# Kernel tuning notes

Measured on AMD Instinct MI355X. Metric: run time of the kernel, lower is better.

## Reference

```python
import jax, jax.numpy as jnp
import numpy as np

N, E, H, IN_NF, G, STEPS, EHID = 4096, 8192, 128, 64, 8, 3, 32


def setup_inputs() -> dict:
    key = jax.random.key(0)
    ks = jax.random.split(key, 24)

    def gn(k, shape, fan_in):
        return jax.random.normal(k, shape, dtype=jnp.float32) / np.sqrt(fan_in)

    inp = {
        "x": jax.random.normal(ks[0], (N, IN_NF), dtype=jnp.float32),
        "edge_index": jax.random.randint(ks[1], (2, E), 0, N, dtype=jnp.int32),
        "edge_attr": jax.random.uniform(ks[2], (E, 1), dtype=jnp.float32),
        "batch": jnp.sort(jax.random.randint(ks[3], (N,), 0, G, dtype=jnp.int32)),
        # lin0: in_nf -> hid
        "lin0_w": gn(ks[4], (IN_NF, H), IN_NF),
        "lin0_b": jnp.zeros((H,), jnp.float32),
        # per-step edge MLP: 1 -> 32 -> H*H (stacked over STEPS)
        "nn_w1": gn(ks[5], (STEPS, 1, EHID), 1),
        "nn_b1": jnp.zeros((STEPS, EHID), jnp.float32),
        "nn_w2": gn(ks[6], (STEPS, EHID, H * H), EHID) * 0.1,
        "nn_b2": jnp.zeros((STEPS, H * H), jnp.float32),
        # NNConv root weight (no bias) + conv bias, per step
        "root_w": gn(ks[7], (STEPS, H, H), H),
        "conv_b": jnp.zeros((STEPS, H), jnp.float32),
        # single-layer GRU (input H, hidden H); gate order r, z, n
        "gru_wih": gn(ks[8], (3 * H, H), H),
        "gru_whh": gn(ks[9], (3 * H, H), H),
        "gru_bih": jnp.zeros((3 * H,), jnp.float32),
        "gru_bhh": jnp.zeros((3 * H,), jnp.float32),
        # readout
        "lin1_w": gn(ks[10], (H, H // 2), H),
        "lin1_b": jnp.zeros((H // 2,), jnp.float32),
        "lin2_w": gn(ks[11], (H // 2, 1), H // 2),
        "lin2_b": jnp.zeros((1,), jnp.float32),
    }
    return inp


def _gru_cell(m, h, wih, whh, bih, bhh):
    gi = m @ wih.T + bih          # [N, 3H]
    gh = h @ whh.T + bhh          # [N, 3H]
    i_r, i_z, i_n = jnp.split(gi, 3, axis=-1)
    h_r, h_z, h_n = jnp.split(gh, 3, axis=-1)
    r = jax.nn.sigmoid(i_r + h_r)
    z = jax.nn.sigmoid(i_z + h_z)
    n = jnp.tanh(i_n + r * h_n)
    return (1.0 - z) * n + z * h


def reference(x, edge_index, edge_attr, batch, lin0_w, lin0_b, nn_w1, nn_b1,
              nn_w2, nn_b2, root_w, conv_b, gru_wih, gru_whh, gru_bih,
              gru_bhh, lin1_w, lin1_b, lin2_w, lin2_b):
    n_nodes = x.shape[0]
    row, col = edge_index[0], edge_index[1]  # source j -> target i

    x = jax.nn.relu(x @ lin0_w + lin0_b)     # [N, H]
    h = x

    # in-degree for mean aggregation (0-degree nodes -> 0 output)
    deg = jax.ops.segment_sum(jnp.ones((row.shape[0],), x.dtype), col,
                              num_segments=n_nodes)
    inv_deg = jnp.where(deg > 0, 1.0 / jnp.maximum(deg, 1.0), 0.0)[:, None]

    for t in range(STEPS):
        # edge-conditioned weights: [E, H, H]
        e_h = jax.nn.relu(edge_attr @ nn_w1[t] + nn_b1[t])
        w_e = (e_h @ nn_w2[t] + nn_b2[t]).reshape(-1, H, H)
        # gather -> per-edge matvec -> scatter-mean
        msg = jnp.einsum('eh,eho->eo', x[row], w_e)
        agg = jax.ops.segment_sum(msg, col, num_segments=n_nodes) * inv_deg
        m = jax.nn.relu(agg + x @ root_w[t] + conv_b[t])
        h = _gru_cell(m, h, gru_wih, gru_whh, gru_bih, gru_bhh)
        x = h

    # global mean pool over graphs
    cnt = jax.ops.segment_sum(jnp.ones((n_nodes,), x.dtype), batch,
                              num_segments=G)
    g = jax.ops.segment_sum(x, batch, num_segments=G) / jnp.maximum(cnt, 1.0)[:, None]
    g = jax.nn.relu(g @ lin1_w + lin1_b)  # dropout: eval mode (identity)
    out = g @ lin2_w + lin2_b             # [G, 1]
    return out
```

## Files before the change

### kernel.cpp

```cpp
#include <hip/hip_runtime.h>
#include <math.h>

#define NN 4096
#define EE 8192
#define HH 128
#define GG 8
#define MU 4096

typedef __attribute__((ext_vector_type(8))) _Float16 half8;
typedef __attribute__((ext_vector_type(4))) float floatx4;

__device__ __forceinline__ void ldst16(const _Float16* g, void* l) {
    __builtin_amdgcn_global_load_lds(
        (const __attribute__((address_space(1))) unsigned int*)g,
        (__attribute__((address_space(3))) unsigned int*)l, 16, 0, 0);
}

__device__ __forceinline__ unsigned f2u(float f) {
    unsigned b = __float_as_uint(f);
    return (b & 0x80000000u) ? ~b : (b | 0x80000000u);
}
__device__ __forceinline__ float u2f(unsigned u) {
    return __uint_as_float((u & 0x80000000u) ? (u ^ 0x80000000u) : ~u);
}

__device__ __forceinline__ int cls_k(float w, float b, float mn, float mx) {
    const float hi = w > 0.f ? w * mx + b : w * mn + b;
    const float lo = w > 0.f ? w * mn + b : w * mx + b;
    if (hi <= 0.f) return 0;
    if (lo >= 0.f) return 1;
    return 2;
}

__global__ __launch_bounds__(256) void ymix_gh_k(
    const _Float16* __restrict__ A, const _Float16* __restrict__ BT3t,
    const _Float16* __restrict__ Bhh, const float* __restrict__ bhh,
    const float* __restrict__ w2t, _Float16* __restrict__ Y,
    float* __restrict__ g2, _Float16* __restrict__ U,
    const int* __restrict__ kflag)
{
    __shared__ __align__(16) _Float16 As[128 * 32];
    __shared__ __align__(16) _Float16 Bs[128 * 32];
    const int tid = threadIdx.x;
    const int lane = tid & 63, wave = tid >> 6;
    const int m0 = blockIdx.y * 128;
    const int wr = (wave >> 1) * 64, wc = (wave & 1) * 64;
    const int fm = lane & 15, fq = lane >> 4;
    const int srow = tid >> 2, soff = (tid & 3) << 3;
    const _Float16* gA0 = A + (size_t)(m0 + srow) * 128 + soff;
    const _Float16* gA1 = gA0 + (size_t)64 * 128;
    char* lA0 = (char*)As + tid * 16;  char* lA1 = (char*)As + (tid + 256) * 16;
    char* lB0 = (char*)Bs + tid * 16;  char* lB1 = (char*)Bs + (tid + 256) * 16;
    const int bx = blockIdx.x;
    const int er = fq * 4, ec = fm;

    floatx4 acc[4][4] = {};
    if (bx < 6) {
        const _Float16* gB0 = (bx < 3)
            ? BT3t + (size_t)(bx * 128 + srow) * 128 + soff
            : Bhh + (size_t)((bx - 3) * 128 + srow) * 128 + soff;
        const _Float16* gB1 = gB0 + (size_t)64 * 128;
        for (int k0 = 0; k0 < 128; k0 += 32) {
            __syncthreads();
            ldst16(gA0 + k0, lA0); ldst16(gA1 + k0, lA1);
            ldst16(gB0 + k0, lB0); ldst16(gB1 + k0, lB1);
            __syncthreads();
            half8 af[4], bf[4];
#pragma unroll
            for (int i = 0; i < 4; ++i)
                af[i] = *(const half8*)&As[(wr + i * 16 + fm) * 32 + fq * 8];
#pragma unroll
            for (int j = 0; j < 4; ++j)
                bf[j] = *(const half8*)&Bs[(wc + j * 16 + fm) * 32 + fq * 8];
#pragma unroll
            for (int i = 0; i < 4; ++i)
#pragma unroll
                for (int j = 0; j < 4; ++j)
                    acc[i][j] = __builtin_amdgcn_mfma_f32_16x16x32_f16(
                        af[i], bf[j], acc[i][j], 0, 0, 0);
        }
        if (bx < 3) {
#pragma unroll
            for (int i = 0; i < 4; ++i) {
                const int gr = m0 + wr + i * 16 + er;
#pragma unroll
                for (int j = 0; j < 4; ++j) {
                    const int gc = bx * 128 + wc + j * 16 + ec;
#pragma unroll
                    for (int r = 0; r < 4; ++r)
                        Y[(size_t)(gr + r) * 384 + gc] = (_Float16)acc[i][j][r];
                }
            }
        } else {
            const int n0 = (bx - 3) * 128;
#pragma unroll
            for (int i = 0; i < 4; ++i) {
                const int gr = m0 + wr + i * 16 + er;
#pragma unroll
                for (int j = 0; j < 4; ++j) {
                    const int gc = n0 + wc + j * 16 + ec;
                    const float bv = bhh[gc];
#pragma unroll
                    for (int r = 0; r < 4; ++r)
                        g2[(size_t)(gr + r) * 384 + gc] = acc[i][j][r] + bv;
                }
            }
        }
    } else {
        const unsigned f = *(const unsigned*)kflag;
        const int kk = bx - 6;
        if (!((f >> kk) & 1u)) return;
        const int cbase = __popc(f & ((1u << kk) - 1u)) << 7;
        const float* w2s = w2t + (size_t)kk * 16384;
        for (int k0 = 0; k0 < 128; k0 += 32) {
            __syncthreads();
            ldst16(gA0 + k0, lA0); ldst16(gA1 + k0, lA1);
#pragma unroll
            for (int c = tid; c < 512; c += 256) {
                const int row = c >> 2, seg = (c & 3) << 3;
                _Float16 v8[8];
#pragma unroll
                for (int u = 0; u < 8; ++u)
                    v8[u] = (_Float16)w2s[(size_t)(k0 + seg + u) * 128 + row];
                *(half8*)&Bs[row * 32 + seg] = *(half8*)v8;
            }
            __syncthreads();
            half8 af[4], bf[4];
#pragma unroll
            for (int i = 0; i < 4; ++i)
                af[i] = *(const half8*)&As[(wr + i * 16 + fm) * 32 + fq * 8];
#pragma unroll
            for (int j = 0; j < 4; ++j)
                bf[j] = *(const half8*)&Bs[(wc + j * 16 + fm) * 32 + fq * 8];
#pragma unroll
            for (int i = 0; i < 4; ++i)
#pragma unroll
                for (int j = 0; j < 4; ++j)
                    acc[i][j] = __builtin_amdgcn_mfma_f32_16x16x32_f16(
                        af[i], bf[j], acc[i][j], 0, 0, 0);
        }
#pragma unroll
        for (int i = 0; i < 4; ++i) {
            const int gr = m0 + wr + i * 16 + er;
#pragma unroll
            for (int j = 0; j < 4; ++j) {
                const int gc = cbase + wc + j * 16 + ec;
#pragma unroll
                for (int r = 0; r < 4; ++r)
                    U[(size_t)(gr + r) * MU + gc] = (_Float16)acc[i][j][r];
            }
        }
    }
}

__global__ __launch_bounds__(256) void escat_k(
    const int2* __restrict__ rc, const float2* __restrict__ ec2,
    const float* __restrict__ ehPt, const _Float16* __restrict__ Y,
    const _Float16* __restrict__ U, float* __restrict__ mpre,
    const int* __restrict__ kflag)
{
    const int b = blockIdx.x;
    const int p0 = ((b & 7) * 512 + (b >> 3)) * 2;
    const int h2 = threadIdx.x >> 7;
    const int o = threadIdx.x & 127;
    const int p = p0 + h2;
    const int2 e = rc[p];
    const float2 c = ec2[p];
    const _Float16* Yr = Y + (size_t)e.x * 384;
    float acc = c.x * (float)Yr[o] + c.y * (float)Yr[128 + o];
    const unsigned f = *(const unsigned*)kflag;
    if (f) {
        const int nk = __popc(f);
        const _Float16* Ur = U + (size_t)e.x * MU;
        const float* ep = ehPt + (size_t)p * 32;
        for (int i = 0; i < nk; ++i)
            acc += ep[i] * (float)Ur[i * 128 + o];
    }
    atomicAdd(&mpre[(size_t)e.y * 128 + o], acc);
}

__global__ __launch_bounds__(256) void gruz0_k(
    const float* __restrict__ mpre, const _Float16* __restrict__ Y,
    const float* __restrict__ cb, const _Float16* __restrict__ Bih,
    const float* __restrict__ bih, float* __restrict__ g1)
{
    __shared__ __align__(16) _Float16 As[128 * 40];
    __shared__ __align__(16) _Float16 Bs[128 * 40];
    const int tid = threadIdx.x;
    const int lane = tid & 63, wave = tid >> 6;
    const int m0 = blockIdx.y * 128, n0 = blockIdx.x * 128;
    const int wr = (wave >> 1) * 64, wc = (wave & 1) * 64;
    const int fm = lane & 15, fq = lane >> 4;

    floatx4 acc[4][4] = {};
    for (int k0 = 0; k0 < 128; k0 += 32) {
        __syncthreads();
#pragma unroll
        for (int c = tid; c < 512; c += 256) {
            const int row = c >> 2, seg = (c & 3) << 3;
            const int mr = m0 + row;
            const half8 yv = *(const half8*)&Y[(size_t)mr * 384 + 256 + k0 + seg];
            const float4 a0 = *(const float4*)&mpre[(size_t)mr * 128 + k0 + seg];
            const float4 a1 = *(const float4*)&mpre[(size_t)mr * 128 + k0 + seg + 4];
            const float4 c0 = *(const float4*)&cb[k0 + seg];
            const float4 c1 = *(const float4*)&cb[k0 + seg + 4];
            _Float16 v8[8];
            float v;
            v = (float)yv[0] + a0.x + c0.x; v8[0] = (_Float16)(v > 0.f ? v : 0.f);
            v = (float)yv[1] + a0.y + c0.y; v8[1] = (_Float16)(v > 0.f ? v : 0.f);
            v = (float)yv[2] + a0.z + c0.z; v8[2] = (_Float16)(v > 0.f ? v : 0.f);
            v = (float)yv[3] + a0.w + c0.w; v8[3] = (_Float16)(v > 0.f ? v : 0.f);
            v = (float)yv[4] + a1.x + c1.x; v8[4] = (_Float16)(v > 0.f ? v : 0.f);
            v = (float)yv[5] + a1.y + c1.y; v8[5] = (_Float16)(v > 0.f ? v : 0.f);
            v = (float)yv[6] + a1.z + c1.z; v8[6] = (_Float16)(v > 0.f ? v : 0.f);
            v = (float)yv[7] + a1.w + c1.w; v8[7] = (_Float16)(v > 0.f ? v : 0.f);
            *(half8*)&As[row * 40 + seg] = *(half8*)v8;
            *(half8*)&Bs[row * 40 + seg] =
                *(const half8*)&Bih[(size_t)(n0 + row) * 128 + k0 + seg];
        }
        __syncthreads();
        half8 af[4], bf[4];
#pragma unroll
        for (int i = 0; i < 4; ++i)
            af[i] = *(const half8*)&As[(wr + i * 16 + fm) * 40 + fq * 8];
#pragma unroll
        for (int j = 0; j < 4; ++j)
            bf[j] = *(const half8*)&Bs[(wc + j * 16 + fm) * 40 + fq * 8];
#pragma unroll
        for (int i = 0; i < 4; ++i)
#pragma unroll
            for (int j = 0; j < 4; ++j)
                acc[i][j] = __builtin_amdgcn_mfma_f32_16x16x32_f16(
                    af[i], bf[j], acc[i][j], 0, 0, 0);
    }
    const int er = fq * 4, ec = fm;
#pragma unroll
    for (int i = 0; i < 4; ++i) {
        const int gr = m0 + wr + i * 16 + er;
#pragma unroll
        for (int j = 0; j < 4; ++j) {
            const int gc = n0 + wc + j * 16 + ec;
            const float bv = bih[gc];
#pragma unroll
            for (int r = 0; r < 4; ++r)
                g1[(size_t)(gr + r) * 384 + gc] = acc[i][j][r] + bv;
        }
    }
}

__global__ void gate_k(const float* __restrict__ G1, const float* __restrict__ G2,
                       float* __restrict__ xh, _Float16* __restrict__ Ax,
                       const int* __restrict__ batch, float* __restrict__ pooled) {
    const int idx = blockIdx.x * 256 + threadIdx.x;
    const int n = idx >> 7, o = idx & 127;
    const size_t b = (size_t)n * 384;
    float ir = G1[b + o], iz = G1[b + 128 + o], in_ = G1[b + 256 + o];
    float hr = G2[b + o], hz = G2[b + 128 + o], hn = G2[b + 256 + o];
    float r = 1.f / (1.f + expf(-(ir + hr)));
    float z = 1.f / (1.f + expf(-(iz + hz)));
    float nv = tanhf(in_ + r * hn);
    float hv = (1.f - z) * nv + z * xh[idx];
    xh[idx] = hv;
    Ax[idx] = (_Float16)hv;
    if (pooled) atomicAdd(&pooled[batch[n] * 128 + o], hv);
}

__global__ __launch_bounds__(256) void setup_lin0_k(
    const float* __restrict__ wih, const float* __restrict__ whh,
    _Float16* __restrict__ Bih, _Float16* __restrict__ Bhh,
    const int* __restrict__ ei, const float* __restrict__ eattr,
    const int* __restrict__ batch,
    float* __restrict__ deg, int* __restrict__ odeg, float* __restrict__ cnt,
    unsigned* __restrict__ eaMM,
    const float* __restrict__ x, const float* __restrict__ l0w,
    const float* __restrict__ l0b, float* __restrict__ xh,
    _Float16* __restrict__ Ax)
{
    __shared__ float loc8[GG];
    __shared__ float As[16][64];
    __shared__ float Bs[16][64];
    const int b = blockIdx.x, t = threadIdx.x;
    if (b < 192) {
        const int idx = b * 256 + t;
        Bih[idx] = (_Float16)wih[idx];
        Bhh[idx] = (_Float16)whh[idx];
    } else if (b < 224) {
        const int e = (b - 192) * 256 + t;
        atomicAdd(&deg[ei[EE + e]], 1.0f);
        atomicAdd(&odeg[ei[e]], 1);
        const float ea = eattr[e];
        unsigned u1 = f2u(ea), u2 = f2u(-ea);
#pragma unroll
        for (int off = 32; off > 0; off >>= 1) {
            unsigned o1 = __shfl_down(u1, off), o2 = __shfl_down(u2, off);
            u1 = u1 > o1 ? u1 : o1;  u2 = u2 > o2 ? u2 : o2;
        }
        if ((t & 63) == 0) { atomicMax(&eaMM[0], u1); atomicMax(&eaMM[1], u2); }
    } else if (b < 240) {
        const int n = (b - 224) * 256 + t;
        if (t < GG) loc8[t] = 0.f;
        __syncthreads();
        atomicAdd(&loc8[batch[n]], 1.0f);
        __syncthreads();
        if (t < GG) atomicAdd(&cnt[t], loc8[t]);
    } else {
        const int bb = b - 240;
        const int j0 = (bb & 1) * 64;
        const int m0 = (bb >> 1) * 64;
        const int tx = t & 15, ty = t >> 4;
        const int arow = t >> 2, acol = (t & 3) << 2;
        const int bk = t >> 4, bj = (t & 15) << 2;
        float c[4][4] = {};
        for (int k0 = 0; k0 < 64; k0 += 16) {
            __syncthreads();
            float4 av = *(const float4*)&x[(size_t)(m0 + arow) * 64 + k0 + acol];
            As[acol + 0][arow] = av.x;
            As[acol + 1][arow] = av.y;
            As[acol + 2][arow] = av.z;
            As[acol + 3][arow] = av.w;
            *(float4*)&Bs[bk][bj] = *(const float4*)&l0w[(size_t)(k0 + bk) * 128 + j0 + bj];
            __syncthreads();
#pragma unroll
            for (int kk = 0; kk < 16; ++kk) {
                const float4 a = *(const float4*)&As[kk][ty << 2];
                const float4 bv = *(const float4*)&Bs[kk][tx << 2];
                c[0][0] += a.x * bv.x; c[0][1] += a.x * bv.y; c[0][2] += a.x * bv.z; c[0][3] += a.x * bv.w;
                c[1][0] += a.y * bv.x; c[1][1] += a.y * bv.y; c[1][2] += a.y * bv.z; c[1][3] += a.y * bv.w;
                c[2][0] += a.z * bv.x; c[2][1] += a.z * bv.y; c[2][2] += a.z * bv.z; c[2][3] += a.z * bv.w;
                c[3][0] += a.w * bv.x; c[3][1] += a.w * bv.y; c[3][2] += a.w * bv.z; c[3][3] += a.w * bv.w;
            }
        }
        const float4 bv = *(const float4*)&l0b[j0 + (tx << 2)];
        const int col0 = j0 + (tx << 2);
#pragma unroll
        for (int i = 0; i < 4; ++i) {
            const int row = m0 + (ty << 2) + i;
            float4 o;
            o.x = fmaxf(c[i][0] + bv.x, 0.f); o.y = fmaxf(c[i][1] + bv.y, 0.f);
            o.z = fmaxf(c[i][2] + bv.z, 0.f); o.w = fmaxf(c[i][3] + bv.w, 0.f);
            *(float4*)&xh[(size_t)row * 128 + col0] = o;
            _Float16* base = Ax + (size_t)row * 128 + col0;
            base[0] = (_Float16)o.x; base[1] = (_Float16)o.y;
            base[2] = (_Float16)o.z; base[3] = (_Float16)o.w;
        }
    }
}

__global__ __launch_bounds__(256) void scan_wsum_k(
    const int* __restrict__ odeg, int* __restrict__ ocur,
    const float* __restrict__ w1, const float* __restrict__ b1,
    const float* __restrict__ w2, const float* __restrict__ b2,
    const float* __restrict__ rw, const unsigned* __restrict__ eaMM,
    _Float16* __restrict__ BT3)
{
    const int t = threadIdx.x;
    if (blockIdx.x == 0) {
        __shared__ int ps[256];
        const int base = t * 16;
        int l[16]; int s = 0;
#pragma unroll
        for (int i = 0; i < 16; ++i) { l[i] = s; s += odeg[base + i]; }
        ps[t] = s;
        __syncthreads();
        for (int d = 1; d < 256; d <<= 1) {
            int v = (t >= d) ? ps[t - d] : 0;
            __syncthreads();
            ps[t] += v;
            __syncthreads();
        }
        const int excl = (t == 0) ? 0 : ps[t - 1];
#pragma unroll
        for (int i = 0; i < 16; ++i) ocur[base + i] = excl + l[i];
    } else {
        __shared__ float wl[32], bl[32];
        const int bb = blockIdx.x - 1;
        const int st = bb >> 6;
        if (t < 32) {
            const float w = w1[st * 32 + t], bv = b1[st * 32 + t];
            const float mx = u2f(eaMM[0]), mn = -u2f(eaMM[1]);
            const int c = cls_k(w, bv, mn, mx);
            wl[t] = (c == 1) ? w : 0.f;
            bl[t] = (c == 1) ? bv : 0.f;
        }
        __syncthreads();
        const int idx = (bb & 63) * 256 + t;
        const int h = idx >> 7, o = idx & 127;
        const float* W2t = w2 + (size_t)st * 524288;
        float a = 0.f, c2 = 0.f;
#pragma unroll 8
        for (int j = 0; j < 32; ++j) {
            const float v = W2t[(size_t)j * 16384 + idx];
            a += wl[j] * v; c2 += bl[j] * v;
        }
        c2 += b2[(size_t)st * 16384 + idx];
        _Float16* B = BT3 + (size_t)st * 49152;
        B[(size_t)o * 128 + h]         = (_Float16)a;
        B[(size_t)(128 + o) * 128 + h] = (_Float16)c2;
        B[(size_t)(256 + o) * 128 + h] = (_Float16)rw[(size_t)st * 16384 + idx];
    }
}

__global__ __launch_bounds__(256) void scatter_k(
    const int* __restrict__ ei, const float* __restrict__ eattr,
    const float* __restrict__ w1, const float* __restrict__ b1,
    const float* __restrict__ deg, int* __restrict__ ocur,
    const unsigned* __restrict__ eaMM,
    int2* __restrict__ rc, float2* __restrict__ ec2,
    float* __restrict__ ehP, int* __restrict__ kflag)
{
    __shared__ unsigned mm[3];
    if (threadIdx.x < 3) mm[threadIdx.x] = 0u;
    __syncthreads();
    if (threadIdx.x < 96) {
        const int tt = threadIdx.x >> 5, k = threadIdx.x & 31;
        const float w = w1[tt * 32 + k], bv = b1[tt * 32 + k];
        const float mx = u2f(eaMM[0]), mn = -u2f(eaMM[1]);
        if (cls_k(w, bv, mn, mx) == 2) atomicOr(&mm[tt], 1u << k);
    }
    __syncthreads();
    const int wave = threadIdx.x >> 6, lane = threadIdx.x & 63;
    const int e = blockIdx.x * 4 + wave;
    const int r = ei[e], c = ei[EE + e];
    int pos = 0;
    if (lane == 0) pos = atomicAdd(&ocur[r], 1);
    pos = __shfl(pos, 0);
    const float d = deg[c];
    const float inv = d > 0.f ? 1.0f / d : 0.0f;
    const float ea = eattr[e];
    if (lane == 0) {
        rc[pos] = make_int2(r, c);
        ec2[pos] = make_float2(ea * inv, inv);
    }
#pragma unroll
    for (int t = 0; t < 3; ++t) {
        const unsigned m = mm[t];
        if (lane < 32 && ((m >> lane) & 1u)) {
            const float v = ea * w1[t * 32 + lane] + b1[t * 32 + lane];
            const int slot = __popc(m & ((1u << lane) - 1u));
            ehP[((size_t)t * EE + pos) * 32 + slot] = (v > 0.f ? v : 0.f) * inv;
        }
    }
    if (threadIdx.x < 3) kflag[threadIdx.x] = (int)mm[threadIdx.x];
}

__global__ __launch_bounds__(128) void final_k(
    const float* __restrict__ pooled, const float* __restrict__ cnt,
    const float* __restrict__ l1w, const float* __restrict__ l1b,
    const float* __restrict__ l2w, const float* __restrict__ l2b,
    float* __restrict__ out)
{
    __shared__ float gv[128];
    const int g = blockIdx.x, t = threadIdx.x;
    float c = cnt[g]; c = c > 1.f ? c : 1.f;
    gv[t] = pooled[g * 128 + t] / c;
    __syncthreads();
    if (t < 64) {
        float y = l1b[t];
        for (int h = 0; h < 128; ++h) y += gv[h] * l1w[h * 64 + t];
        y = y > 0.f ? y : 0.f;
        float s = y * l2w[t];
#pragma unroll
        for (int off = 32; off > 0; off >>= 1)
            s += __shfl_down(s, off);
        if (t == 0) out[g] = s + l2b[0];
    }
}

extern "C" void kernel_launch(void* const* d_in, const int* in_sizes, int n_in,
                              void* d_out, int out_size, void* d_ws, size_t ws_size,
                              hipStream_t stream) {
    const float* x      = (const float*)d_in[0];
    const int*   ei     = (const int*)d_in[1];
    const float* eattr  = (const float*)d_in[2];
    const int*   batch  = (const int*)d_in[3];
    const float* lin0_w = (const float*)d_in[4];
    const float* lin0_b = (const float*)d_in[5];
    const float* nn_w1  = (const float*)d_in[6];
    const float* nn_b1  = (const float*)d_in[7];
    const float* nn_w2  = (const float*)d_in[8];
    const float* nn_b2  = (const float*)d_in[9];
    const float* root_w = (const float*)d_in[10];
    const float* conv_b = (const float*)d_in[11];
    const float* gwih   = (const float*)d_in[12];
    const float* gwhh   = (const float*)d_in[13];
    const float* gbih   = (const float*)d_in[14];
    const float* gbhh   = (const float*)d_in[15];
    const float* l1w    = (const float*)d_in[16];
    const float* l1b    = (const float*)d_in[17];
    const float* l2w    = (const float*)d_in[18];
    const float* l2b    = (const float*)d_in[19];
    float* out = (float*)d_out;
    float* ws  = (float*)d_ws;

    float*    mpre0  = ws;
    float*    pooled = ws + 1572864;
    float*    cnt    = ws + 1573888;
    float*    deg    = ws + 1573896;
    int*      odeg   = (int*)(ws + 1577992);
    unsigned* eaMM   = (unsigned*)(ws + 1582088);
    int*      kflag  = (int*)(ws + 1582090);
    int*      ocur   = (int*)(ws + 1582096);
    int2*     rc     = (int2*)(ws + 1586192);
    float2*   ec2    = (float2*)(ws + 1602576);
    float*    ehP    = ws + 1618960;
    float*    xh     = ws + 2405392;
    float*    g1     = ws + 2929680;
    float*    g2     = ws + 4502544;
    _Float16* Y      = (_Float16*)(ws + 6075408);
    _Float16* U      = (_Float16*)(ws + 6861840);
    _Float16* Ax     = (_Float16*)(ws + 15250448);
    _Float16* BT3    = (_Float16*)(ws + 15512592);
    _Float16* Bih16  = (_Float16*)(ws + 15586320);
    _Float16* Bhh16  = (_Float16*)(ws + 15610896);

    hipMemsetAsync(mpre0, 0, 6328384, stream);
    setup_lin0_k<<<368, 256, 0, stream>>>(gwih, gwhh, Bih16, Bhh16, ei, eattr,
                                          batch, deg, odeg, cnt, eaMM,
                                          x, lin0_w, lin0_b, xh, Ax);
    scan_wsum_k<<<193, 256, 0, stream>>>(odeg, ocur, nn_w1, nn_b1, nn_w2,
                                         nn_b2, root_w, eaMM, BT3);
    scatter_k<<<2048, 256, 0, stream>>>(ei, eattr, nn_w1, nn_b1, deg, ocur,
                                        eaMM, rc, ec2, ehP, kflag);

    for (int t = 0; t < 3; ++t) {
        float* mpre = mpre0 + (size_t)t * 524288;
        ymix_gh_k<<<dim3(38, 32), 256, 0, stream>>>(
            Ax, BT3 + (size_t)t * 49152, Bhh16, gbhh,
            nn_w2 + (size_t)t * 524288, Y, g2, U, kflag + t);
        escat_k<<<4096, 256, 0, stream>>>(rc, ec2, ehP + (size_t)t * EE * 32,
                                          Y, U, mpre, kflag + t);
        gruz0_k<<<dim3(3, 32), 256, 0, stream>>>(mpre, Y, conv_b + t * 128,
                                                 Bih16, gbih, g1);
        gate_k<<<2048, 256, 0, stream>>>(g1, g2, xh, Ax, batch,
                                         (t == 2) ? pooled : nullptr);
    }

    final_k<<<GG, 128, 0, stream>>>(pooled, cnt, l1w, l1b, l2w, l2b, out);
}
```

Baseline: 215.0 us.

## Fuse per-step GRU message-passing kernels into one persistent kernel with grid barriers

Replaces the 13 per-step launches (ymix_gh, escat, gruz0, gate, final) with a single persistent mega-kernel that loops over the three steps, uses grid-stride work distribution, and separates phases with an atomic-counter grid barrier. It also zeroes mpre inside the kernel instead of with a large memset. The goal is to remove launch overhead and inter-kernel gaps, at the cost of spin-barrier overhead, reduced parallelism in small phases, and a deadlock risk if not all blocks are co-resident. The grid size comes from an occupancy query, capped at 4 blocks per unit, and assumes 256 compute units.

```diff
diff --git a/kernel.cpp b/kernel.cpp
--- a/kernel.cpp
+++ b/kernel.cpp
@@ -32,237 +32,278 @@
     return 2;
 }
 
-__global__ __launch_bounds__(256) void ymix_gh_k(
-    const _Float16* __restrict__ A, const _Float16* __restrict__ BT3t,
-    const _Float16* __restrict__ Bhh, const float* __restrict__ bhh,
-    const float* __restrict__ w2t, _Float16* __restrict__ Y,
-    float* __restrict__ g2, _Float16* __restrict__ U,
-    const int* __restrict__ kflag)
+__device__ __forceinline__ void gbar(unsigned* bar, unsigned target) {
+    __syncthreads();
+    if (threadIdx.x == 0) {
+        __threadfence();
+        atomicAdd(bar, 1u);
+        while (atomicAdd(bar, 0u) < target)
+            __builtin_amdgcn_s_sleep(2);
+        __threadfence();
+    }
+    __syncthreads();
+}
+
+__global__ __launch_bounds__(256) void mega_k(
+    const int2* __restrict__ rc, const float2* __restrict__ ec2,
+    const float* __restrict__ ehP, const _Float16* __restrict__ BT3,
+    const _Float16* __restrict__ Bih, const _Float16* __restrict__ Bhh,
+    const float* __restrict__ bih, const float* __restrict__ bhh,
+    const float* __restrict__ conv_b, const float* __restrict__ w2,
+    _Float16* __restrict__ Y, _Float16* __restrict__ U,
+    float* __restrict__ mpre0, float* __restrict__ g1, float* __restrict__ g2,
+    float* __restrict__ xh, _Float16* __restrict__ Ax,
+    const int* __restrict__ batch, float* __restrict__ pooled,
+    const int* __restrict__ kflag, const float* __restrict__ cnt,
+    const float* __restrict__ l1w, const float* __restrict__ l1b,
+    const float* __restrict__ l2w, const float* __restrict__ l2b,
+    float* __restrict__ out, unsigned* __restrict__ bar)
 {
-    __shared__ __align__(16) _Float16 As[128 * 32];
-    __shared__ __align__(16) _Float16 Bs[128 * 32];
+    __shared__ __align__(16) _Float16 S1[128 * 40];
+    __shared__ __align__(16) _Float16 S2[128 * 40];
     const int tid = threadIdx.x;
     const int lane = tid & 63, wave = tid >> 6;
-    const int m0 = blockIdx.y * 128;
     const int wr = (wave >> 1) * 64, wc = (wave & 1) * 64;
     const int fm = lane & 15, fq = lane >> 4;
-    const int srow = tid >> 2, soff = (tid & 3) << 3;
-    const _Float16* gA0 = A + (size_t)(m0 + srow) * 128 + soff;
-    const _Float16* gA1 = gA0 + (size_t)64 * 128;
-    char* lA0 = (char*)As + tid * 16;  char* lA1 = (char*)As + (tid + 256) * 16;
-    char* lB0 = (char*)Bs + tid * 16;  char* lB1 = (char*)Bs + (tid + 256) * 16;
-    const int bx = blockIdx.x;
     const int er = fq * 4, ec = fm;
-
-    floatx4 acc[4][4] = {};
-    if (bx < 6) {
-        const _Float16* gB0 = (bx < 3)
-            ? BT3t + (size_t)(bx * 128 + srow) * 128 + soff
-            : Bhh + (size_t)((bx - 3) * 128 + srow) * 128 + soff;
-        const _Float16* gB1 = gB0 + (size_t)64 * 128;
-        for (int k0 = 0; k0 < 128; k0 += 32) {
-            __syncthreads();
-            ldst16(gA0 + k0, lA0); ldst16(gA1 + k0, lA1);
-            ldst16(gB0 + k0, lB0); ldst16(gB1 + k0, lB1);
-            __syncthreads();
-            half8 af[4], bf[4];
-#pragma unroll
-            for (int i = 0; i < 4; ++i)
-                af[i] = *(const half8*)&As[(wr + i * 16 + fm) * 32 + fq * 8];
-#pragma unroll
-            for (int j = 0; j < 4; ++j)
-                bf[j] = *(const half8*)&Bs[(wc + j * 16 + fm) * 32 + fq * 8];
-#pragma unroll
-            for (int i = 0; i < 4; ++i)
+    const int nb = gridDim.x;
+    unsigned tgt = 0;
+
+    for (int t = 0; t < 3; ++t) {
+        const unsigned f = ((const unsigned*)kflag)[t];
+        const _Float16* BT3t = BT3 + (size_t)t * 49152;
+        const float* cb = conv_b + t * 128;
+        const float* ehPt = ehP + (size_t)t * EE * 32;
+        const float* w2t = w2 + (size_t)t * 524288;
+        float* mpre = mpre0 + (size_t)t * 524288;
+
+        for (int u = blockIdx.x; u < 192; u += nb) {
+            const int bx = u % 6, by = u / 6;
+            const int m0 = by * 128;
+            const int srow = tid >> 2, soff = (tid & 3) << 3;
+            const _Float16* gA0 = Ax + (size_t)(m0 + srow) * 128 + soff;
+            const _Float16* gA1 = gA0 + (size_t)64 * 128;
+            char* lA0 = (char*)S1 + tid * 16; char* lA1 = (char*)S1 + (tid + 256) * 16;
+            char* lB0 = (char*)S2 + tid * 16; char* lB1 = (char*)S2 + (tid + 256) * 16;
+            const _Float16* gB0 = (bx < 3)
+                ? BT3t + (size_t)(bx * 128 + srow) * 128 + soff
+                : Bhh + (size_t)((bx - 3) * 128 + srow) * 128 + soff;
+            const _Float16* gB1 = gB0 + (size_t)64 * 128;
+            floatx4 acc[4][4] = {};
+            for (int k0 = 0; k0 < 128; k0 += 32) {
+                __syncthreads();
+                ldst16(gA0 + k0, lA0); ldst16(gA1 + k0, lA1);
+                ldst16(gB0 + k0, lB0); ldst16(gB1 + k0, lB1);
+                __syncthreads();
+                half8 af[4], bf[4];
+#pragma unroll
+                for (int i = 0; i < 4; ++i)
+                    af[i] = *(const half8*)&S1[(wr + i * 16 + fm) * 32 + fq * 8];
 #pragma unroll
                 for (int j = 0; j < 4; ++j)
-                    acc[i][j] = __builtin_amdgcn_mfma_f32_16x16x32_f16(
-                        af[i], bf[j], acc[i][j], 0, 0, 0);
-        }
-        if (bx < 3) {
+                    bf[j] = *(const half8*)&S2[(wc + j * 16 + fm) * 32 + fq * 8];
+#pragma unroll
+                for (int i = 0; i < 4; ++i)
+#pragma unroll
+                    for (int j = 0; j < 4; ++j)
+                        acc[i][j] = __builtin_amdgcn_mfma_f32_16x16x32_f16(
+                            af[i], bf[j], acc[i][j], 0, 0, 0);
+            }
+            if (bx < 3) {
+#pragma unroll
+                for (int i = 0; i < 4; ++i) {
+                    const int gr = m0 + wr + i * 16 + er;
+#pragma unroll
+                    for (int j = 0; j < 4; ++j) {
+                        const int gc = bx * 128 + wc + j * 16 + ec;
+#pragma unroll
+                        for (int r = 0; r < 4; ++r)
+                            Y[(size_t)(gr + r) * 384 + gc] = (_Float16)acc[i][j][r];
+                    }
+                }
+            } else {
+                const int n0 = (bx - 3) * 128;
+#pragma unroll
+                for (int i = 0; i < 4; ++i) {
+                    const int gr = m0 + wr + i * 16 + er;
+#pragma unroll
+                    for (int j = 0; j < 4; ++j) {
+                        const int gc = n0 + wc + j * 16 + ec;
+                        const float bv = bhh[gc];
+#pragma unroll
+                        for (int r = 0; r < 4; ++r)
+                            g2[(size_t)(gr + r) * 384 + gc] = acc[i][j][r] + bv;
+                    }
+                }
+            }
+        }
+        if (f) {
+            for (int u = blockIdx.x; u < 1024; u += nb) {
+                const int kk = u & 31, by = u >> 5;
+                if (!((f >> kk) & 1u)) continue;
+                const int cbase = __popc(f & ((1u << kk) - 1u)) << 7;
+                const int m0 = by * 128;
+                const int srow = tid >> 2, soff = (tid & 3) << 3;
+                const _Float16* gA0 = Ax + (size_t)(m0 + srow) * 128 + soff;
+                const _Float16* gA1 = gA0 + (size_t)64 * 128;
+                char* lA0 = (char*)S1 + tid * 16; char* lA1 = (char*)S1 + (tid + 256) * 16;
+                const float* w2s = w2t + (size_t)kk * 16384;
+                floatx4 acc[4][4] = {};
+                for (int k0 = 0; k0 < 128; k0 += 32) {
+                    __syncthreads();
+                    ldst16(gA0 + k0, lA0); ldst16(gA1 + k0, lA1);
+#pragma unroll
+                    for (int c = tid; c < 512; c += 256) {
+                        const int row = c >> 2, seg = (c & 3) << 3;
+                        _Float16 v8[8];
+#pragma unroll
+                        for (int uu = 0; uu < 8; ++uu)
+                            v8[uu] = (_Float16)w2s[(size_t)(k0 + seg + uu) * 128 + row];
+                        *(half8*)&S2[row * 32 + seg] = *(half8*)v8;
+                    }
+                    __syncthreads();
+                    half8 af[4], bf[4];
+#pragma unroll
+                    for (int i = 0; i < 4; ++i)
+                        af[i] = *(const half8*)&S1[(wr + i * 16 + fm) * 32 + fq * 8];
+#pragma unroll
+                    for (int j = 0; j < 4; ++j)
+                        bf[j] = *(const half8*)&S2[(wc + j * 16 + fm) * 32 + fq * 8];
+#pragma unroll
+                    for (int i = 0; i < 4; ++i)
+#pragma unroll
+                        for (int j = 0; j < 4; ++j)
+                            acc[i][j] = __builtin_amdgcn_mfma_f32_16x16x32_f16(
+                                af[i], bf[j], acc[i][j], 0, 0, 0);
+                }
+#pragma unroll
+                for (int i = 0; i < 4; ++i) {
+                    const int gr = m0 + wr + i * 16 + er;
+#pragma unroll
+                    for (int j = 0; j < 4; ++j) {
+                        const int gc = cbase + wc + j * 16 + ec;
+#pragma unroll
+                        for (int r = 0; r < 4; ++r)
+                            U[(size_t)(gr + r) * MU + gc] = (_Float16)acc[i][j][r];
+                    }
+                }
+            }
+        }
+        for (int i = blockIdx.x * 256 + tid; i < 131072; i += nb * 256)
+            ((float4*)mpre)[i] = make_float4(0.f, 0.f, 0.f, 0.f);
+        tgt += nb; gbar(bar, tgt);
+
+        for (int i = blockIdx.x * 256 + tid; i < EE * 128; i += nb * 256) {
+            const int u = i >> 8, h2 = (i >> 7) & 1, o = i & 127;
+            const int p = ((u & 7) * 512 + (u >> 3)) * 2 + h2;
+            const int2 e = rc[p];
+            const float2 c = ec2[p];
+            const _Float16* Yr = Y + (size_t)e.x * 384;
+            float acc = c.x * (float)Yr[o] + c.y * (float)Yr[128 + o];
+            if (f) {
+                const int nk = __popc(f);
+                const _Float16* Ur = U + (size_t)e.x * MU;
+                const float* ep = ehPt + (size_t)p * 32;
+                for (int q = 0; q < nk; ++q)
+                    acc += ep[q] * (float)Ur[q * 128 + o];
+            }
+            atomicAdd(&mpre[(size_t)e.y * 128 + o], acc);
+        }
+        tgt += nb; gbar(bar, tgt);
+
+        for (int u = blockIdx.x; u < 96; u += nb) {
+            const int n0 = (u % 3) * 128, m0 = (u / 3) * 128;
+            floatx4 acc[4][4] = {};
+            for (int k0 = 0; k0 < 128; k0 += 32) {
+                __syncthreads();
+#pragma unroll
+                for (int c = tid; c < 512; c += 256) {
+                    const int row = c >> 2, seg = (c & 3) << 3;
+                    const int mr = m0 + row;
+                    const half8 yv = *(const half8*)&Y[(size_t)mr * 384 + 256 + k0 + seg];
+                    const float4 a0 = *(const float4*)&mpre[(size_t)mr * 128 + k0 + seg];
+                    const float4 a1 = *(const float4*)&mpre[(size_t)mr * 128 + k0 + seg + 4];
+                    const float4 c0 = *(const float4*)&cb[k0 + seg];
+                    const float4 c1 = *(const float4*)&cb[k0 + seg + 4];
+                    _Float16 v8[8];
+                    float v;
+                    v = (float)yv[0] + a0.x + c0.x; v8[0] = (_Float16)(v > 0.f ? v : 0.f);
+                    v = (float)yv[1] + a0.y + c0.y; v8[1] = (_Float16)(v > 0.f ? v : 0.f);
+                    v = (float)yv[2] + a0.z + c0.z; v8[2] = (_Float16)(v > 0.f ? v : 0.f);
+                    v = (float)yv[3] + a0.w + c0.w; v8[3] = (_Float16)(v > 0.f ? v : 0.f);
+                    v = (float)yv[4] + a1.x + c1.x; v8[4] = (_Float16)(v > 0.f ? v : 0.f);
+                    v = (float)yv[5] + a1.y + c1.y; v8[5] = (_Float16)(v > 0.f ? v : 0.f);
+                    v = (float)yv[6] + a1.z + c1.z; v8[6] = (_Float16)(v > 0.f ? v : 0.f);
+                    v = (float)yv[7] + a1.w + c1.w; v8[7] = (_Float16)(v > 0.f ? v : 0.f);
+                    *(half8*)&S1[row * 40 + seg] = *(half8*)v8;
+                    *(half8*)&S2[row * 40 + seg] =
+                        *(const half8*)&Bih[(size_t)(n0 + row) * 128 + k0 + seg];
+                }
+                __syncthreads();
+                half8 af[4], bf[4];
+#pragma unroll
+                for (int i = 0; i < 4; ++i)
+                    af[i] = *(const half8*)&S1[(wr + i * 16 + fm) * 40 + fq * 8];
+#pragma unroll
+                for (int j = 0; j < 4; ++j)
+                    bf[j] = *(const half8*)&S2[(wc + j * 16 + fm) * 40 + fq * 8];
+#pragma unroll
+                for (int i = 0; i < 4; ++i)
+#pragma unroll
+                    for (int j = 0; j < 4; ++j)
+                        acc[i][j] = __builtin_amdgcn_mfma_f32_16x16x32_f16(
+                            af[i], bf[j], acc[i][j], 0, 0, 0);
+            }
 #pragma unroll
             for (int i = 0; i < 4; ++i) {
                 const int gr = m0 + wr + i * 16 + er;
 #pragma unroll
                 for (int j = 0; j < 4; ++j) {
-                    const int gc = bx * 128 + wc + j * 16 + ec;
+                    const int gc = n0 + wc + j * 16 + ec;
+                    const float bv = bih[gc];
 #pragma unroll
                     for (int r = 0; r < 4; ++r)
-                        Y[(size_t)(gr + r) * 384 + gc] = (_Float16)acc[i][j][r];
+                        g1[(size_t)(gr + r) * 384 + gc] = acc[i][j][r] + bv;
                 }
             }
-        } else {
-            const int n0 = (bx - 3) * 128;
-#pragma unroll
-            for (int i = 0; i < 4; ++i) {
-                const int gr = m0 + wr + i * 16 + er;
-#pragma unroll
-                for (int j = 0; j < 4; ++j) {
-                    const int gc = n0 + wc + j * 16 + ec;
-                    const float bv = bhh[gc];
-#pragma unroll
-                    for (int r = 0; r < 4; ++r)
-                        g2[(size_t)(gr + r) * 384 + gc] = acc[i][j][r] + bv;
-                }
-            }
-        }
-    } else {
-        const unsigned f = *(const unsigned*)kflag;
-        const int kk = bx - 6;
-        if (!((f >> kk) & 1u)) return;
-        const int cbase = __popc(f & ((1u << kk) - 1u)) << 7;
-        const float* w2s = w2t + (size_t)kk * 16384;
-        for (int k0 = 0; k0 < 128; k0 += 32) {
-            __syncthreads();
-            ldst16(gA0 + k0, lA0); ldst16(gA1 + k0, lA1);
-#pragma unroll
-            for (int c = tid; c < 512; c += 256) {
-                const int row = c >> 2, seg = (c & 3) << 3;
-                _Float16 v8[8];
-#pragma unroll
-                for (int u = 0; u < 8; ++u)
-                    v8[u] = (_Float16)w2s[(size_t)(k0 + seg + u) * 128 + row];
-                *(half8*)&Bs[row * 32 + seg] = *(half8*)v8;
-            }
-            __syncthreads();
-            half8 af[4], bf[4];
-#pragma unroll
-            for (int i = 0; i < 4; ++i)
-                af[i] = *(const half8*)&As[(wr + i * 16 + fm) * 32 + fq * 8];
-#pragma unroll
-            for (int j = 0; j < 4; ++j)
-                bf[j] = *(const half8*)&Bs[(wc + j * 16 + fm) * 32 + fq * 8];
-#pragma unroll
-            for (int i = 0; i < 4; ++i)
-#pragma unroll
-                for (int j = 0; j < 4; ++j)
-                    acc[i][j] = __builtin_amdgcn_mfma_f32_16x16x32_f16(
-                        af[i], bf[j], acc[i][j], 0, 0, 0);
-        }
-#pragma unroll
-        for (int i = 0; i < 4; ++i) {
-            const int gr = m0 + wr + i * 16 + er;
-#pragma unroll
-            for (int j = 0; j < 4; ++j) {
-                const int gc = cbase + wc + j * 16 + ec;
-#pragma unroll
-                for (int r = 0; r < 4; ++r)
-                    U[(size_t)(gr + r) * MU + gc] = (_Float16)acc[i][j][r];
-            }
-        }
-    }
-}
-
-__global__ __launch_bounds__(256) void escat_k(
-    const int2* __restrict__ rc, const float2* __restrict__ ec2,
-    const float* __restrict__ ehPt, const _Float16* __restrict__ Y,
-    const _Float16* __restrict__ U, float* __restrict__ mpre,
-    const int* __restrict__ kflag)
-{
-    const int b = blockIdx.x;
-    const int p0 = ((b & 7) * 512 + (b >> 3)) * 2;
-    const int h2 = threadIdx.x >> 7;
-    const int o = threadIdx.x & 127;
-    const int p = p0 + h2;
-    const int2 e = rc[p];
-    const float2 c = ec2[p];
-    const _Float16* Yr = Y + (size_t)e.x * 384;
-    float acc = c.x * (float)Yr[o] + c.y * (float)Yr[128 + o];
-    const unsigned f = *(const unsigned*)kflag;
-    if (f) {
-        const int nk = __popc(f);
-        const _Float16* Ur = U + (size_t)e.x * MU;
-        const float* ep = ehPt + (size_t)p * 32;
-        for (int i = 0; i < nk; ++i)
-            acc += ep[i] * (float)Ur[i * 128 + o];
-    }
-    atomicAdd(&mpre[(size_t)e.y * 128 + o], acc);
-}
-
-__global__ __launch_bounds__(256) void gruz0_k(
-    const float* __restrict__ mpre, const _Float16* __restrict__ Y,
-    const float* __restrict__ cb, const _Float16* __restrict__ Bih,
-    const float* __restrict__ bih, float* __restrict__ g1)
-{
-    __shared__ __align__(16) _Float16 As[128 * 40];
-    __shared__ __align__(16) _Float16 Bs[128 * 40];
-    const int tid = threadIdx.x;
-    const int lane = tid & 63, wave = tid >> 6;
-    const int m0 = blockIdx.y * 128, n0 = blockIdx.x * 128;
-    const int wr = (wave >> 1) * 64, wc = (wave & 1) * 64;
-    const int fm = lane & 15, fq = lane >> 4;
-
-    floatx4 acc[4][4] = {};
-    for (int k0 = 0; k0 < 128; k0 += 32) {
+        }
+        tgt += nb; gbar(bar, tgt);
+
+        for (int i = blockIdx.x * 256 + tid; i < NN * 128; i += nb * 256) {
+            const int n = i >> 7, o = i & 127;
+            const size_t b = (size_t)n * 384;
+            float ir = g1[b + o], iz = g1[b + 128 + o], in_ = g1[b + 256 + o];
+            float hr = g2[b + o], hz = g2[b + 128 + o], hn = g2[b + 256 + o];
+            float r = 1.f / (1.f + expf(-(ir + hr)));
+            float z = 1.f / (1.f + expf(-(iz + hz)));
+            float nv = tanhf(in_ + r * hn);
+            float hv = (1.f - z) * nv + z * xh[i];
+            xh[i] = hv;
+            Ax[i] = (_Float16)hv;
+            if (t == 2) atomicAdd(&pooled[batch[n] * 128 + o], hv);
+        }
+        tgt += nb; gbar(bar, tgt);
+    }
+
+    for (int g = blockIdx.x; g < GG; g += nb) {
+        float* gv = (float*)S1;
+        if (tid < 128) {
+            float c = cnt[g]; c = c > 1.f ? c : 1.f;
+            gv[tid] = pooled[g * 128 + tid] / c;
+        }
         __syncthreads();
-#pragma unroll
-        for (int c = tid; c < 512; c += 256) {
-            const int row = c >> 2, seg = (c & 3) << 3;
-            const int mr = m0 + row;
-            const half8 yv = *(const half8*)&Y[(size_t)mr * 384 + 256 + k0 + seg];
-            const float4 a0 = *(const float4*)&mpre[(size_t)mr * 128 + k0 + seg];
-            const float4 a1 = *(const float4*)&mpre[(size_t)mr * 128 + k0 + seg + 4];
-            const float4 c0 = *(const float4*)&cb[k0 + seg];
-            const float4 c1 = *(const float4*)&cb[k0 + seg + 4];
-            _Float16 v8[8];
-            float v;
-            v = (float)yv[0] + a0.x + c0.x; v8[0] = (_Float16)(v > 0.f ? v : 0.f);
-            v = (float)yv[1] + a0.y + c0.y; v8[1] = (_Float16)(v > 0.f ? v : 0.f);
-            v = (float)yv[2] + a0.z + c0.z; v8[2] = (_Float16)(v > 0.f ? v : 0.f);
-            v = (float)yv[3] + a0.w + c0.w; v8[3] = (_Float16)(v > 0.f ? v : 0.f);
-            v = (float)yv[4] + a1.x + c1.x; v8[4] = (_Float16)(v > 0.f ? v : 0.f);
-            v = (float)yv[5] + a1.y + c1.y; v8[5] = (_Float16)(v > 0.f ? v : 0.f);
-            v = (float)yv[6] + a1.z + c1.z; v8[6] = (_Float16)(v > 0.f ? v : 0.f);
-            v = (float)yv[7] + a1.w + c1.w; v8[7] = (_Float16)(v > 0.f ? v : 0.f);
-            *(half8*)&As[row * 40 + seg] = *(half8*)v8;
-            *(half8*)&Bs[row * 40 + seg] =
-                *(const half8*)&Bih[(size_t)(n0 + row) * 128 + k0 + seg];
+        if (tid < 64) {
+            float y = l1b[tid];
+            for (int h = 0; h < 128; ++h) y += gv[h] * l1w[h * 64 + tid];
+            y = y > 0.f ? y : 0.f;
+            float s = y * l2w[tid];
+#pragma unroll
+            for (int off = 32; off > 0; off >>= 1)
+                s += __shfl_down(s, off);
+            if (tid == 0) out[g] = s + l2b[0];
         }
         __syncthreads();
-        half8 af[4], bf[4];
-#pragma unroll
-        for (int i = 0; i < 4; ++i)
-            af[i] = *(const half8*)&As[(wr + i * 16 + fm) * 40 + fq * 8];
-#pragma unroll
-        for (int j = 0; j < 4; ++j)
-            bf[j] = *(const half8*)&Bs[(wc + j * 16 + fm) * 40 + fq * 8];
-#pragma unroll
-        for (int i = 0; i < 4; ++i)
-#pragma unroll
-            for (int j = 0; j < 4; ++j)
-                acc[i][j] = __builtin_amdgcn_mfma_f32_16x16x32_f16(
-                    af[i], bf[j], acc[i][j], 0, 0, 0);
-    }
-    const int er = fq * 4, ec = fm;
-#pragma unroll
-    for (int i = 0; i < 4; ++i) {
-        const int gr = m0 + wr + i * 16 + er;
-#pragma unroll
-        for (int j = 0; j < 4; ++j) {
-            const int gc = n0 + wc + j * 16 + ec;
-            const float bv = bih[gc];
-#pragma unroll
-            for (int r = 0; r < 4; ++r)
-                g1[(size_t)(gr + r) * 384 + gc] = acc[i][j][r] + bv;
-        }
-    }
-}
-
-__global__ void gate_k(const float* __restrict__ G1, const float* __restrict__ G2,
-                       float* __restrict__ xh, _Float16* __restrict__ Ax,
-                       const int* __restrict__ batch, float* __restrict__ pooled) {
-    const int idx = blockIdx.x * 256 + threadIdx.x;
-    const int n = idx >> 7, o = idx & 127;
-    const size_t b = (size_t)n * 384;
-    float ir = G1[b + o], iz = G1[b + 128 + o], in_ = G1[b + 256 + o];
-    float hr = G2[b + o], hz = G2[b + 128 + o], hn = G2[b + 256 + o];
-    float r = 1.f / (1.f + expf(-(ir + hr)));
-    float z = 1.f / (1.f + expf(-(iz + hz)));
-    float nv = tanhf(in_ + r * hn);
-    float hv = (1.f - z) * nv + z * xh[idx];
-    xh[idx] = hv;
-    Ax[idx] = (_Float16)hv;
-    if (pooled) atomicAdd(&pooled[batch[n] * 128 + o], hv);
+    }
 }
 
 __global__ __launch_bounds__(256) void setup_lin0_k(
@@ -443,29 +484,6 @@
     if (threadIdx.x < 3) kflag[threadIdx.x] = (int)mm[threadIdx.x];
 }
 
-__global__ __launch_bounds__(128) void final_k(
-    const float* __restrict__ pooled, const float* __restrict__ cnt,
-    const float* __restrict__ l1w, const float* __restrict__ l1b,
-    const float* __restrict__ l2w, const float* __restrict__ l2b,
-    float* __restrict__ out)
-{
-    __shared__ float gv[128];
-    const int g = blockIdx.x, t = threadIdx.x;
-    float c = cnt[g]; c = c > 1.f ? c : 1.f;
-    gv[t] = pooled[g * 128 + t] / c;
-    __syncthreads();
-    if (t < 64) {
-        float y = l1b[t];
-        for (int h = 0; h < 128; ++h) y += gv[h] * l1w[h * 64 + t];
-        y = y > 0.f ? y : 0.f;
-        float s = y * l2w[t];
-#pragma unroll
-        for (int off = 32; off > 0; off >>= 1)
-            s += __shfl_down(s, off);
-        if (t == 0) out[g] = s + l2b[0];
-    }
-}
-
 extern "C" void kernel_launch(void* const* d_in, const int* in_sizes, int n_in,
                               void* d_out, int out_size, void* d_ws, size_t ws_size,
                               hipStream_t stream) {
@@ -492,28 +510,29 @@
     float* out = (float*)d_out;
     float* ws  = (float*)d_ws;
 
-    float*    mpre0  = ws;
-    float*    pooled = ws + 1572864;
-    float*    cnt    = ws + 1573888;
-    float*    deg    = ws + 1573896;
-    int*      odeg   = (int*)(ws + 1577992);
-    unsigned* eaMM   = (unsigned*)(ws + 1582088);
-    int*      kflag  = (int*)(ws + 1582090);
-    int*      ocur   = (int*)(ws + 1582096);
-    int2*     rc     = (int2*)(ws + 1586192);
-    float2*   ec2    = (float2*)(ws + 1602576);
-    float*    ehP    = ws + 1618960;
-    float*    xh     = ws + 2405392;
-    float*    g1     = ws + 2929680;
-    float*    g2     = ws + 4502544;
+    float*    pooled = ws;
+    float*    cnt    = ws + 1024;
+    float*    deg    = ws + 1032;
+    int*      odeg   = (int*)(ws + 5128);
+    unsigned* eaMM   = (unsigned*)(ws + 9224);
+    int*      kflag  = (int*)(ws + 9226);
+    unsigned* bar    = (unsigned*)(ws + 9229);
+    int*      ocur   = (int*)(ws + 9232);
+    int2*     rc     = (int2*)(ws + 13328);
+    float2*   ec2    = (float2*)(ws + 29712);
+    float*    ehP    = ws + 46096;
+    float*    xh     = ws + 832528;
+    float*    g1     = ws + 1356816;
+    float*    g2     = ws + 2929680;
+    float*    mpre0  = ws + 4502544;
     _Float16* Y      = (_Float16*)(ws + 6075408);
-    _Float16* U      = (_Float16*)(ws + 6861840);
-    _Float16* Ax     = (_Float16*)(ws + 15250448);
-    _Float16* BT3    = (_Float16*)(ws + 15512592);
-    _Float16* Bih16  = (_Float16*)(ws + 15586320);
-    _Float16* Bhh16  = (_Float16*)(ws + 15610896);
-
-    hipMemsetAsync(mpre0, 0, 6328384, stream);
+    _Float16* Ax     = (_Float16*)(ws + 6861840);
+    _Float16* BT3    = (_Float16*)(ws + 7123984);
+    _Float16* Bih16  = (_Float16*)(ws + 7197712);
+    _Float16* Bhh16  = (_Float16*)(ws + 7222288);
+    _Float16* U      = (_Float16*)(ws + 7246864);
+
+    hipMemsetAsync(pooled, 0, 36928, stream);
     setup_lin0_k<<<368, 256, 0, stream>>>(gwih, gwhh, Bih16, Bhh16, ei, eattr,
                                           batch, deg, odeg, cnt, eaMM,
                                           x, lin0_w, lin0_b, xh, Ax);
@@ -522,18 +541,15 @@
     scatter_k<<<2048, 256, 0, stream>>>(ei, eattr, nn_w1, nn_b1, deg, ocur,
                                         eaMM, rc, ec2, ehP, kflag);
 
-    for (int t = 0; t < 3; ++t) {
-        float* mpre = mpre0 + (size_t)t * 524288;
-        ymix_gh_k<<<dim3(38, 32), 256, 0, stream>>>(
-            Ax, BT3 + (size_t)t * 49152, Bhh16, gbhh,
-            nn_w2 + (size_t)t * 524288, Y, g2, U, kflag + t);
-        escat_k<<<4096, 256, 0, stream>>>(rc, ec2, ehP + (size_t)t * EE * 32,
-                                          Y, U, mpre, kflag + t);
-        gruz0_k<<<dim3(3, 32), 256, 0, stream>>>(mpre, Y, conv_b + t * 128,
-                                                 Bih16, gbih, g1);
-        gate_k<<<2048, 256, 0, stream>>>(g1, g2, xh, Ax, batch,
-                                         (t == 2) ? pooled : nullptr);
-    }
-
-    final_k<<<GG, 128, 0, stream>>>(pooled, cnt, l1w, l1b, l2w, l2b, out);
-}
+    static int maxb = 0;
+    if (maxb == 0) {
+        if (hipOccupancyMaxActiveBlocksPerMultiprocessor(&maxb, mega_k, 256, 0)
+                != hipSuccess || maxb < 1)
+            maxb = 1;
+        if (maxb > 4) maxb = 4;
+    }
+    mega_k<<<maxb * 256, 256, 0, stream>>>(
+        rc, ec2, ehP, BT3, Bih16, Bhh16, gbih, gbhh, conv_b, nn_w2,
+        Y, U, mpre0, g1, g2, xh, Ax, batch, pooled, kflag,
+        cnt, l1w, l1b, l2w, l2b, out, bar);
+}
```

Result: slower. 495.3 us (+130.4%).
